# Kernel optimization log

Measured on AMD Instinct MI355X. Metric: run time of the kernel, lower is better.

The kernel has to match this reference:

```python
import jax, jax.numpy as jnp
import numpy as np

GAMMA = 0.1   # sdtw_gamma from train_config
WARP = 1.0    # sdtw_warp from train_config
BIG = 1e8     # stand-in for +inf in the DP table (safe in fp32 logsumexp)


def soft_dtw(D, gamma, warp):
    """SoftDTW with warp penalty via anti-diagonal wavefront DP.

    D: [B, N, M] pairwise cost matrix. Returns [B] soft-DTW values.
    Recurrence: R[i,j] = D[i,j] + softmin_gamma(R[i-1,j-1], R[i-1,j]+warp, R[i,j-1]+warp)
    """
    B, N, M = D.shape
    R = jnp.full((B, N + 1, M + 1), BIG, D.dtype)
    R = R.at[:, 0, 0].set(0.0)
    ii = jnp.arange(N)  # cell row indices on a diagonal

    def body(R, k):
        jj = k - ii                       # cell col indices, i+j = k
        valid = (jj >= 0) & (jj < M)
        jc = jnp.clip(jj, 0, M - 1)
        # padded-coordinate predecessors of cell (ii, jj)
        r_diag = R[:, ii, jc]             # R[i-1, j-1]
        r_up = R[:, ii, jc + 1] + warp    # R[i-1, j] + warp
        r_left = R[:, ii + 1, jc] + warp  # R[i, j-1] + warp
        stacked = jnp.stack([r_diag, r_up, r_left], axis=0)  # [3, B, N]
        smin = -gamma * jax.nn.logsumexp(-stacked / gamma, axis=0)
        new = D[:, ii, jc] + smin
        cur = R[:, ii + 1, jc + 1]
        upd = jnp.where(valid[None, :], new, cur)
        # row indices ii+1 are all distinct -> no scatter collisions
        R = R.at[:, ii + 1, jc + 1].set(upd)
        return R, None

    R, _ = jax.lax.scan(body, R, jnp.arange(N + M - 1))
    return R[:, N, M]


def setup_inputs() -> dict:
    key = jax.random.key(0)
    k1, k2, k3, k4 = jax.random.split(key, 4)
    mel_pred = jax.random.normal(k1, (4, 512, 80), dtype=jnp.float32)
    mel_target = jax.random.normal(k2, (4, 512, 80), dtype=jnp.float32)
    log_d_pred = jax.random.normal(k3, (4, 128), dtype=jnp.float32)
    d_target = jax.random.randint(k4, (4, 128), 0, 20)
    return {"mel_pred": mel_pred, "mel_target": mel_target,
            "log_d_pred": log_d_pred, "d_target": d_target}


def reference(mel_pred, mel_target, log_d_pred, d_target):
    B, T, _ = mel_pred.shape
    # pairwise L1 frame distance: D[b,i,j] = sum_m |pred[b,i,m] - tgt[b,j,m]|
    D = jnp.abs(mel_pred[:, :, None, :] - mel_target[:, None, :, :]).sum(-1)
    sdtw = soft_dtw(D, GAMMA, WARP)           # [B]
    mel_loss = (sdtw / T).mean()
    # L1 (reduction='none' -> mean) on log-durations
    log_d_target = jnp.log(d_target.astype(jnp.float32) + 1.0)
    duration_loss = jnp.abs(log_d_pred - log_d_target).mean()
    return mel_loss + duration_loss
```

## Files before the change

kernel.cpp:

```cpp
#include <hip/hip_runtime.h>
#include <hip/hip_bf16.h>
#include <hip/hip_fp16.h>
#include <math.h>

#define BIGF 1e8f
#define BIGS 28672.0f

__device__ inline float min3f(float a, float b, float c) {
    float d;
    asm("v_min3_f32 %0, %1, %2, %3" : "=v"(d) : "v"(a), "v"(b), "v"(c));
    return d;
}

__global__ __launch_bounds__(256) void prep_kernel(
        const float* __restrict__ pred, const float* __restrict__ targ,
        __half* __restrict__ Dh) {
    const int bid = blockIdx.x;
    const int t   = threadIdx.x;

    if (bid < 256) {
        const int b  = bid >> 6;
        const int i0 = ((bid >> 3) & 7) * 64;
        const int j0 = (bid & 7) * 64;
        __shared__ float sp[64][81];
        __shared__ float st[64][81];

        const float4* __restrict__ p4 = (const float4*)(pred + ((size_t)b * 512 + i0) * 80);
        const float4* __restrict__ t4 = (const float4*)(targ + ((size_t)b * 512 + j0) * 80);
        #pragma unroll
        for (int q = 0; q < 5; ++q) {
            int idx = q * 256 + t;
            int r = idx / 20, dq = idx % 20;
            float4 v = p4[r * 20 + dq];
            sp[r][dq*4+0]=v.x; sp[r][dq*4+1]=v.y; sp[r][dq*4+2]=v.z; sp[r][dq*4+3]=v.w;
            float4 w = t4[r * 20 + dq];
            st[r][dq*4+0]=w.x; st[r][dq*4+1]=w.y; st[r][dq*4+2]=w.z; st[r][dq*4+3]=w.w;
        }
        __syncthreads();

        const int tx = t & 15, ty = t >> 4;
        float acc[4][4];
        #pragma unroll
        for (int r = 0; r < 4; ++r)
            #pragma unroll
            for (int c = 0; c < 4; ++c) acc[r][c] = 0.f;

        #pragma unroll 4
        for (int d = 0; d < 80; ++d) {
            float a0 = sp[4*ty+0][d], a1 = sp[4*ty+1][d], a2 = sp[4*ty+2][d], a3 = sp[4*ty+3][d];
            float b0 = st[4*tx+0][d], b1 = st[4*tx+1][d], b2 = st[4*tx+2][d], b3 = st[4*tx+3][d];
            acc[0][0] += fabsf(a0-b0); acc[0][1] += fabsf(a0-b1); acc[0][2] += fabsf(a0-b2); acc[0][3] += fabsf(a0-b3);
            acc[1][0] += fabsf(a1-b0); acc[1][1] += fabsf(a1-b1); acc[1][2] += fabsf(a1-b2); acc[1][3] += fabsf(a1-b3);
            acc[2][0] += fabsf(a2-b0); acc[2][1] += fabsf(a2-b1); acc[2][2] += fabsf(a2-b2); acc[2][3] += fabsf(a2-b3);
            acc[3][0] += fabsf(a3-b0); acc[3][1] += fabsf(a3-b1); acc[3][2] += fabsf(a3-b2); acc[3][3] += fabsf(a3-b3);
        }

        #pragma unroll
        for (int r = 0; r < 4; ++r) {
            #pragma unroll
            for (int c = 0; c < 4; ++c) {
                int i = i0 + 4*ty + r;
                int j = j0 + 4*tx + c;
                float v = acc[r][c];
                float w = ((i | j) == 0) ? v : (v + 2.0f);
                Dh[((size_t)b * 1023 + (i + j)) * 512 + i] = __float2half(w);
            }
        }
    } else {
        const int k  = bid - 256;
        const int lo = (k > 511) ? (k - 511) : 0;
        const int hi = (k < 511) ? k : 511;
        const __half big = __float2half(BIGS);
        #pragma unroll
        for (int b = 0; b < 4; ++b) {
            __half* row = Dh + ((size_t)b * 1023 + k) * 512;
            int i1 = t;
            int i2 = t + 256;
            if (i1 < lo || i1 > hi) row[i1] = big;
            if (i2 < lo || i2 > hi) row[i2] = big;
        }
    }
}

#define DPPSHR(x) __int_as_float(__builtin_amdgcn_update_dpp(                 \
        __float_as_int(BIGF), __float_as_int(x), 0x138, 0xF, 0xF, false))

#define STEP(V1, V2, P)                                                       \
  {                                                                           \
    const __half2* hp_ = (const __half2*)&(P);                                \
    float2 f0_ = __half22float2(hp_[0]);                                      \
    float2 f1_ = __half22float2(hp_[1]);                                      \
    float2 f2_ = __half22float2(hp_[2]);                                      \
    float2 f3_ = __half22float2(hp_[3]);                                      \
    float nb1 = DPPSHR(V1[7]);                                                \
    float nb2 = DPPSHR(V2[7]);                                                \
    V2[7] = f3_.y + min3f(V2[6], V1[6], V1[7]);                               \
    V2[6] = f3_.x + min3f(V2[5], V1[5], V1[6]);                               \
    V2[5] = f2_.y + min3f(V2[4], V1[4], V1[5]);                               \
    V2[4] = f2_.x + min3f(V2[3], V1[3], V1[4]);                               \
    V2[3] = f1_.y + min3f(V2[2], V1[2], V1[3]);                               \
    V2[2] = f1_.x + min3f(V2[1], V1[1], V1[2]);                               \
    V2[1] = f0_.y + min3f(V2[0], V1[0], V1[1]);                               \
    V2[0] = f0_.x + min3f(nb2,   nb1,   V1[0]);                               \
  }

__global__ __launch_bounds__(128, 1) void dp_kernel(
        const __half* __restrict__ Dh,
        const float* __restrict__ ldp, const int* __restrict__ dt,
        float* __restrict__ out) {
    const int tid = threadIdx.x;
    if (tid >= 64) {
        if (blockIdx.x == 0) {
            const int l = tid - 64;
            float s = 0.f;
            #pragma unroll
            for (int q = 0; q < 8; ++q) {
                int idx = l * 8 + q;
                s += fabsf(ldp[idx] - logf((float)dt[idx] + 1.0f));
            }
            #pragma unroll
            for (int o = 32; o > 0; o >>= 1) s += __shfl_down(s, o);
            if (l == 0) atomicAdd(out, s * (1.0f / 512.0f));
        }
        return;
    }

    const int b    = blockIdx.x;
    const int lane = tid;
    const char* __restrict__ base = (const char*)(Dh + (size_t)b * 1023 * 512);
    const unsigned loff = (unsigned)lane * 16u;

    float A[8], B[8];
    #pragma unroll
    for (int r = 0; r < 8; ++r) { A[r] = BIGF; B[r] = BIGF; }

    {
        uint4 q0 = *(const uint4*)(base + loff);
        float c00 = __half2float(*(const __half*)&q0.x);
        B[0] = (lane == 0) ? c00 : BIGF;
    }

    uint4 P[16];
    #pragma unroll
    for (int p = 0; p < 16; ++p)
        P[p] = *(const uint4*)(base + (size_t)(1 + p) * 1024 + loff);

    int k0 = 1;
    for (int t = 0; t < 63; ++t, k0 += 16) {
#define PH(p, Vx, Vy)                                                         \
        STEP(Vx, Vy, P[p])                                                    \
        P[p] = *(const uint4*)(base + (size_t)(k0 + 16 + p) * 1024 + loff);
        PH(0,B,A)  PH(1,A,B)  PH(2,B,A)  PH(3,A,B)
        PH(4,B,A)  PH(5,A,B)  PH(6,B,A)  PH(7,A,B)
        PH(8,B,A)  PH(9,A,B)  PH(10,B,A) PH(11,A,B)
        PH(12,B,A) PH(13,A,B) PH(14,B,A) PH(15,A,B)
#undef PH
    }
    STEP(B,A,P[0])  STEP(A,B,P[1])  STEP(B,A,P[2])  STEP(A,B,P[3])
    STEP(B,A,P[4])  STEP(A,B,P[5])  STEP(B,A,P[6])  STEP(A,B,P[7])
    STEP(B,A,P[8])  STEP(A,B,P[9])  STEP(B,A,P[10]) STEP(A,B,P[11])
    STEP(B,A,P[12]) STEP(A,B,P[13])

    if (lane == 63) atomicAdd(out, (B[7] - 1022.0f) * (1.0f / 2048.0f));
}

extern "C" void kernel_launch(void* const* d_in, const int* in_sizes, int n_in,
                              void* d_out, int out_size, void* d_ws, size_t ws_size,
                              hipStream_t stream) {
    const float* pred = (const float*)d_in[0];
    const float* targ = (const float*)d_in[1];
    const float* ldp  = (const float*)d_in[2];
    const int*   dt   = (const int*)d_in[3];
    float* out = (float*)d_out;

    __half* Dh = (__half*)d_ws;

    hipMemsetAsync(out, 0, sizeof(float), stream);
    prep_kernel<<<256 + 1023, 256, 0, stream>>>(pred, targ, Dh);
    dp_kernel<<<4, 128, 0, stream>>>(Dh, ldp, dt, out);
}
```

Baseline: 77.95 us.

## Deepen DP prefetch to 32 diagonals with inline-asm loads and fused half-add

Measured after the change: 73.12 us. 1.07x faster.

```diff
diff --git a/kernel.cpp b/kernel.cpp
--- a/kernel.cpp
+++ b/kernel.cpp
@@ -9,6 +9,18 @@
 __device__ inline float min3f(float a, float b, float c) {
     float d;
     asm("v_min3_f32 %0, %1, %2, %3" : "=v"(d) : "v"(a), "v"(b), "v"(c));
+    return d;
+}
+__device__ inline float addh_lo(unsigned pw, float c) {
+    float d;
+    asm("v_fma_mix_f32 %0, %1, 1.0, %2 op_sel:[0,0,0] op_sel_hi:[1,0,0]"
+        : "=v"(d) : "v"(pw), "v"(c));
+    return d;
+}
+__device__ inline float addh_hi(unsigned pw, float c) {
+    float d;
+    asm("v_fma_mix_f32 %0, %1, 1.0, %2 op_sel:[1,0,0] op_sel_hi:[1,0,0]"
+        : "=v"(d) : "v"(pw), "v"(c));
     return d;
 }
 
@@ -85,23 +97,18 @@
 #define DPPSHR(x) __int_as_float(__builtin_amdgcn_update_dpp(                 \
         __float_as_int(BIGF), __float_as_int(x), 0x138, 0xF, 0xF, false))
 
-#define STEP(V1, V2, P)                                                       \
+#define STEP(V1, V2, Q)                                                       \
   {                                                                           \
-    const __half2* hp_ = (const __half2*)&(P);                                \
-    float2 f0_ = __half22float2(hp_[0]);                                      \
-    float2 f1_ = __half22float2(hp_[1]);                                      \
-    float2 f2_ = __half22float2(hp_[2]);                                      \
-    float2 f3_ = __half22float2(hp_[3]);                                      \
     float nb1 = DPPSHR(V1[7]);                                                \
     float nb2 = DPPSHR(V2[7]);                                                \
-    V2[7] = f3_.y + min3f(V2[6], V1[6], V1[7]);                               \
-    V2[6] = f3_.x + min3f(V2[5], V1[5], V1[6]);                               \
-    V2[5] = f2_.y + min3f(V2[4], V1[4], V1[5]);                               \
-    V2[4] = f2_.x + min3f(V2[3], V1[3], V1[4]);                               \
-    V2[3] = f1_.y + min3f(V2[2], V1[2], V1[3]);                               \
-    V2[2] = f1_.x + min3f(V2[1], V1[1], V1[2]);                               \
-    V2[1] = f0_.y + min3f(V2[0], V1[0], V1[1]);                               \
-    V2[0] = f0_.x + min3f(nb2,   nb1,   V1[0]);                               \
+    V2[7] = addh_hi(Q.w, min3f(V2[6], V1[6], V1[7]));                         \
+    V2[6] = addh_lo(Q.w, min3f(V2[5], V1[5], V1[6]));                         \
+    V2[5] = addh_hi(Q.z, min3f(V2[4], V1[4], V1[5]));                         \
+    V2[4] = addh_lo(Q.z, min3f(V2[3], V1[3], V1[4]));                         \
+    V2[3] = addh_hi(Q.y, min3f(V2[2], V1[2], V1[3]));                         \
+    V2[2] = addh_lo(Q.y, min3f(V2[1], V1[1], V1[2]));                         \
+    V2[1] = addh_hi(Q.x, min3f(V2[0], V1[0], V1[1]));                         \
+    V2[0] = addh_lo(Q.x, min3f(nb2,   nb1,   V1[0]));                         \
   }
 
 __global__ __launch_bounds__(128, 1) void dp_kernel(
@@ -128,38 +135,55 @@
     const int b    = blockIdx.x;
     const int lane = tid;
     const char* __restrict__ base = (const char*)(Dh + (size_t)b * 1023 * 512);
-    const unsigned loff = (unsigned)lane * 16u;
 
     float A[8], B[8];
     #pragma unroll
     for (int r = 0; r < 8; ++r) { A[r] = BIGF; B[r] = BIGF; }
 
     {
-        uint4 q0 = *(const uint4*)(base + loff);
-        float c00 = __half2float(*(const __half*)&q0.x);
+        float c00 = __half2float(*(const __half*)base);
         B[0] = (lane == 0) ? c00 : BIGF;
     }
-
-    uint4 P[16];
+    __builtin_amdgcn_sched_barrier(0);
+
+    unsigned voff = (unsigned)lane * 16u + 1024u;
+    uint4 P[32];
     #pragma unroll
-    for (int p = 0; p < 16; ++p)
-        P[p] = *(const uint4*)(base + (size_t)(1 + p) * 1024 + loff);
-
-    int k0 = 1;
-    for (int t = 0; t < 63; ++t, k0 += 16) {
+    for (int p = 0; p < 32; ++p) {
+        asm volatile("global_load_dwordx4 %0, %1, %2"
+                     : "=v"(P[p]) : "v"(voff), "s"(base) : "memory");
+        voff += 1024u;
+    }
+
+    for (int t = 0; t < 31; ++t) {
 #define PH(p, Vx, Vy)                                                         \
+        asm volatile("s_waitcnt vmcnt(31)" ::: "memory");                     \
+        __builtin_amdgcn_sched_barrier(0);                                    \
         STEP(Vx, Vy, P[p])                                                    \
-        P[p] = *(const uint4*)(base + (size_t)(k0 + 16 + p) * 1024 + loff);
-        PH(0,B,A)  PH(1,A,B)  PH(2,B,A)  PH(3,A,B)
-        PH(4,B,A)  PH(5,A,B)  PH(6,B,A)  PH(7,A,B)
-        PH(8,B,A)  PH(9,A,B)  PH(10,B,A) PH(11,A,B)
-        PH(12,B,A) PH(13,A,B) PH(14,B,A) PH(15,A,B)
+        asm volatile("global_load_dwordx4 %0, %1, %2"                         \
+                     : "=v"(P[p]) : "v"(voff), "s"(base) : "memory");         \
+        voff += 1024u;
+        PH(0,B,A)   PH(1,A,B)   PH(2,B,A)   PH(3,A,B)
+        PH(4,B,A)   PH(5,A,B)   PH(6,B,A)   PH(7,A,B)
+        PH(8,B,A)   PH(9,A,B)   PH(10,B,A)  PH(11,A,B)
+        PH(12,B,A)  PH(13,A,B)  PH(14,B,A)  PH(15,A,B)
+        PH(16,B,A)  PH(17,A,B)  PH(18,B,A)  PH(19,A,B)
+        PH(20,B,A)  PH(21,A,B)  PH(22,B,A)  PH(23,A,B)
+        PH(24,B,A)  PH(25,A,B)  PH(26,B,A)  PH(27,A,B)
+        PH(28,B,A)  PH(29,A,B)  PH(30,B,A)  PH(31,A,B)
 #undef PH
     }
-    STEP(B,A,P[0])  STEP(A,B,P[1])  STEP(B,A,P[2])  STEP(A,B,P[3])
-    STEP(B,A,P[4])  STEP(A,B,P[5])  STEP(B,A,P[6])  STEP(A,B,P[7])
-    STEP(B,A,P[8])  STEP(A,B,P[9])  STEP(B,A,P[10]) STEP(A,B,P[11])
-    STEP(B,A,P[12]) STEP(A,B,P[13])
+
+    asm volatile("s_waitcnt vmcnt(0)" ::: "memory");
+    __builtin_amdgcn_sched_barrier(0);
+    STEP(B,A,P[0])   STEP(A,B,P[1])   STEP(B,A,P[2])   STEP(A,B,P[3])
+    STEP(B,A,P[4])   STEP(A,B,P[5])   STEP(B,A,P[6])   STEP(A,B,P[7])
+    STEP(B,A,P[8])   STEP(A,B,P[9])   STEP(B,A,P[10])  STEP(A,B,P[11])
+    STEP(B,A,P[12])  STEP(A,B,P[13])  STEP(B,A,P[14])  STEP(A,B,P[15])
+    STEP(B,A,P[16])  STEP(A,B,P[17])  STEP(B,A,P[18])  STEP(A,B,P[19])
+    STEP(B,A,P[20])  STEP(A,B,P[21])  STEP(B,A,P[22])  STEP(A,B,P[23])
+    STEP(B,A,P[24])  STEP(A,B,P[25])  STEP(B,A,P[26])  STEP(A,B,P[27])
+    STEP(B,A,P[28])  STEP(A,B,P[29])
 
     if (lane == 63) atomicAdd(out, (B[7] - 1022.0f) * (1.0f / 2048.0f));
 }
```
